# Kernel optimization log

Hardware: AMD Instinct MI355X
Metric: run time of the kernel (lower is better)

## Reference

```python
import jax, jax.numpy as jnp
import numpy as np
from jax.scipy.special import logsumexp

EPSILON = 0.01        # temperature
DIST_THRESH = 0.2
NUM_ITERS = 3
NEG_INF = -1.0e9

B, N, M, C = 4, 4096, 4096, 256


def setup_inputs() -> dict:
    key = jax.random.key(0)
    k1, k2, k3, k4, k5 = jax.random.split(key, 5)
    source_feats = jax.random.normal(k1, (B, N, C), dtype=jnp.float32)
    source_locs = jax.random.uniform(k2, (B, N, 2), dtype=jnp.float32)
    target_locs = jax.random.uniform(k3, (B, M, 2), dtype=jnp.float32)
    source_valid_mask = jax.random.bernoulli(k4, 0.9, (B, N))
    target_valid_mask = jax.random.bernoulli(k5, 0.9, (B, M))
    return {
        "source_feats": source_feats,
        "source_locs": source_locs,
        "target_locs": target_locs,
        "source_valid_mask": source_valid_mask,
        "target_valid_mask": target_valid_mask,
    }


def reference(source_feats, source_locs, target_locs, source_valid_mask, target_valid_mask):
    # pairwise squared distances: [B, M, N]
    diff = target_locs[:, :, None, :] - source_locs[:, None, :, :]  # [B, M, N, 2]
    dist_sq = jnp.sum(diff * diff, axis=-1)                          # [B, M, N]
    log_K = -dist_sq / (EPSILON + 1e-8)

    valid_connection = dist_sq < (DIST_THRESH ** 2)
    valid_connection = valid_connection & source_valid_mask[:, None, :]
    valid_connection = valid_connection & target_valid_mask[:, :, None]
    log_K = jnp.where(valid_connection, log_K, NEG_INF)

    # Sinkhorn iterations in log space
    v = jnp.zeros((log_K.shape[0], 1, log_K.shape[2]), dtype=log_K.dtype)  # [B,1,N]
    u = jnp.zeros((log_K.shape[0], log_K.shape[1], 1), dtype=log_K.dtype)  # [B,M,1]
    for _ in range(NUM_ITERS):
        u = -logsumexp(log_K + v, axis=2, keepdims=True)
        v = -logsumexp(log_K + u, axis=1, keepdims=True)
        v = jnp.where(source_valid_mask[:, None, :], v, 0.0)

    attn = jnp.exp(log_K + u + v)  # [B, M, N]
    attn = jax.lax.stop_gradient(attn)  # original computes it under torch.no_grad

    target_feats = jnp.einsum('bmn,bnc->bmc', attn, source_feats)
    target_feats = target_feats * target_valid_mask[:, :, None].astype(target_feats.dtype)
    has_source = jnp.any(valid_connection, axis=-1, keepdims=True)
    target_feats = target_feats * has_source.astype(target_feats.dtype)
    return target_feats
```

## Files before the change

kernel.cpp:

```cpp
#include <hip/hip_runtime.h>
#include <math.h>

#define BB 4
#define BN 4096
#define CC 256
constexpr float T2      = 0.04f;
constexpr float NEGINF  = -1.0e9f;
constexpr float INV_EPS = (float)(1.0 / 0.01000001);

__device__ __forceinline__ int cell_of(float x, float y) {
  int cx = (int)(x * 5.0f); cx = cx < 0 ? 0 : (cx > 4 ? 4 : cx);
  int cy = (int)(y * 5.0f); cy = cy < 0 ? 0 : (cy > 4 ? 4 : cy);
  return cy * 5 + cx;
}

__global__ void k_count(const float* __restrict__ tlocs, const float* __restrict__ slocs,
                        int* __restrict__ counts_t, int* __restrict__ counts_s) {
  int gid = blockIdx.x * 256 + threadIdx.x;
  if (gid < BB * BN) {
    int b = gid >> 12;
    atomicAdd(&counts_t[b * 32 + cell_of(tlocs[gid * 2], tlocs[gid * 2 + 1])], 1);
  } else {
    int g = gid - BB * BN;
    int b = g >> 12;
    atomicAdd(&counts_s[b * 32 + cell_of(slocs[g * 2], slocs[g * 2 + 1])], 1);
  }
}

__global__ void k_scan_scatter(const float* __restrict__ tlocs, const float* __restrict__ slocs,
                               const int* __restrict__ tmask, const int* __restrict__ smask,
                               const int* __restrict__ counts_t, const int* __restrict__ counts_s,
                               int* __restrict__ starts_t, int* __restrict__ starts_s,
                               int* __restrict__ perm_t, int* __restrict__ perm_s,
                               float4* __restrict__ t_sorted, float4* __restrict__ s_sorted) {
  const int which = blockIdx.x & 1, b = blockIdx.x >> 1;
  const float* locs = which ? slocs : tlocs;
  const int*   mask = which ? smask : tmask;
  const int* counts = which ? counts_s : counts_t;
  int* starts       = which ? starts_s : starts_t;
  int* perm         = which ? perm_s : perm_t;
  float4* pack      = which ? s_sorted : t_sorted;
  __shared__ int st[26];
  __shared__ int cur[25];
  if (threadIdx.x == 0) {
    int acc = 0;
    for (int c = 0; c < 25; c++) { st[c] = acc; acc += counts[b * 32 + c]; }
    st[25] = acc;
  }
  __syncthreads();
  if (threadIdx.x < 25) cur[threadIdx.x] = st[threadIdx.x];
  if (threadIdx.x < 26) starts[b * 32 + threadIdx.x] = st[threadIdx.x];
  __syncthreads();
  for (int i = threadIdx.x; i < BN; i += 256) {
    float x = locs[(b * BN + i) * 2], y = locs[(b * BN + i) * 2 + 1];
    int pos = atomicAdd(&cur[cell_of(x, y)], 1);
    perm[b * BN + pos] = i;
    pack[b * BN + pos] = make_float4(x, y, 0.f, mask[b * BN + i] ? 1.f : 0.f);
  }
}

__global__ __launch_bounds__(256) void k_sink(const float4* __restrict__ opp,
                                              float4* __restrict__ own,
                                              const int* __restrict__ opp_starts,
                                              const int* __restrict__ Zin,
                                              int* __restrict__ Zout,
                                              int zero_invalid) {
  const int row  = blockIdx.x * 4 + (threadIdx.x >> 6);
  const int b    = row >> 12;
  const int lane = threadIdx.x & 63;
  const float4 me = own[row];
  float mrun = -1e30f, srun = 0.f;
  if (me.w != 0.f) {
    const int cell = cell_of(me.x, me.y);
    const int cy = cell / 5, cx = cell % 5;
    const int ry0 = max(cy - 1, 0), ry1 = min(cy + 1, 4);
    const int rx0 = max(cx - 1, 0), rx1 = min(cx + 1, 4);
    for (int ry = ry0; ry <= ry1; ry++) {
      const int r0 = opp_starts[b * 32 + ry * 5 + rx0];
      const int r1 = opp_starts[b * 32 + ry * 5 + rx1 + 1];
      for (int j = r0 + lane; j < r1; j += 64) {
        float4 o = opp[b * BN + j];
        float dx = me.x - o.x, dy = me.y - o.y;
        float d2 = fmaf(dx, dx, dy * dy);
        bool  c  = (d2 < T2) && (o.w != 0.f);
        float t  = c ? fmaf(d2, -INV_EPS, o.z) : -3e30f;
        float d  = t - mrun;
        float e  = __expf(-fabsf(d));
        if (d > 0.f) { srun = fmaf(srun, e, 1.f); mrun = t; }
        else         { srun += e; }
      }
    }
  }
  for (int off = 32; off > 0; off >>= 1) {
    float om = __shfl_down(mrun, off);
    float os = __shfl_down(srun, off);
    float nm = fmaxf(mrun, om);
    srun = srun * __expf(mrun - nm) + os * __expf(om - nm);
    mrun = nm;
  }
  if (lane == 0) {
    const int Z = Zin[b];
    float m0 = mrun, s = srun;
    if (Z > 0) {
      m0 = fmaxf(mrun, 0.f);
      s  = srun * __expf(mrun - m0) + (float)Z * __expf(-m0);
    }
    float val = (s > 0.f) ? -(m0 + logf(s)) : 1.0e9f;
    if (zero_invalid && me.w == 0.f) val = 0.f;
    own[row] = make_float4(me.x, me.y, val, me.w);
    if (val == 1.0e9f) atomicAdd(&Zout[b], 1);
  }
}

#define MAXCH 12

__global__ __launch_bounds__(256) void k_out(
    const float* __restrict__ feats, const float4* __restrict__ t_sorted,
    const float4* __restrict__ s_sorted, const int* __restrict__ perm_t,
    const int* __restrict__ perm_s, const int* __restrict__ starts_t,
    const int* __restrict__ starts_s, float* __restrict__ out) {
  const int b = blockIdx.z;
  const int cell = blockIdx.y / 3, rsel = blockIdx.y % 3;
  const int cy = cell / 5, cx = cell % 5;
  const int ry = cy + rsel - 1;
  if (ry < 0 || ry > 4) return;
  const int t0 = starts_t[b * 32 + cell], t1 = starts_t[b * 32 + cell + 1];
  const int base = t0 + blockIdx.x * 32;
  if (base >= t1) return;
  const int rx0 = max(cx - 1, 0), rx1 = min(cx + 1, 4);
  const int s0 = starts_s[b * 32 + ry * 5 + rx0];
  const int s1 = starts_s[b * 32 + ry * 5 + rx1 + 1];
  if (s0 >= s1) return;
  const int nt = min(32, t1 - base);

  __shared__ float4 tL[32];
  __shared__ int    morg[32];
  __shared__ float4 sL[16];
  __shared__ int    sorg[16];
  __shared__ __align__(16) float attnL[16][32];
  __shared__ __align__(16) float fL[16 * 256];

  const int tid = threadIdx.x;
  if (tid < 32) {
    if (tid < nt) {
      tL[tid]   = t_sorted[b * BN + base + tid];
      morg[tid] = perm_t[b * BN + base + tid];
    } else {
      tL[tid]   = make_float4(0.f, 0.f, 0.f, 0.f);
      morg[tid] = 0;
    }
  }
  const int tmg = tid >> 5;
  const int chg = tid & 31;
  float acc[4][8];
  #pragma unroll
  for (int i = 0; i < 4; i++)
    #pragma unroll
    for (int j = 0; j < 8; j++) acc[i][j] = 0.f;
  __syncthreads();

  for (int n0 = s0; n0 < s1; n0 += 16) {
    const int kk = min(16, s1 - n0);
    __syncthreads();
    if (tid < 16) {
      if (tid < kk) {
        sL[tid]   = s_sorted[b * BN + n0 + tid];
        sorg[tid] = perm_s[b * BN + n0 + tid];
      } else {
        sL[tid]   = make_float4(1e9f, 1e9f, 0.f, 0.f);
        sorg[tid] = 0;
      }
    }
    __syncthreads();
    {
      int e = tid * 2;
      #pragma unroll
      for (int q = 0; q < 2; q++, e++) {
        int nn = e >> 5, tm = e & 31;
        float4 t4 = tL[tm];
        float4 s4 = sL[nn];
        float dx = t4.x - s4.x, dy = t4.y - s4.y;
        float d2 = fmaf(dx, dx, dy * dy);
        bool  c  = (d2 < T2) && (s4.w != 0.f) && (t4.w != 0.f);
        attnL[nn][tm] = c ? __expf(fmaf(d2, -INV_EPS, t4.z + s4.z)) : 0.f;
      }
    }
    #pragma unroll
    for (int q = 0; q < 4; q++) {
      int idx = q * 256 + tid;
      ((float4*)fL)[idx] =
          ((const float4*)feats)[(((b << 12) + sorg[idx >> 6]) << 6) + (idx & 63)];
    }
    __syncthreads();
    #pragma unroll 4
    for (int nn = 0; nn < 16; nn++) {
      const float4 av = *(const float4*)&attnL[nn][tmg * 4];
      const float4 f0 = *(const float4*)&fL[nn * 256 + chg * 4];
      const float4 f1 = *(const float4*)&fL[nn * 256 + 128 + chg * 4];
      float avv[4] = {av.x, av.y, av.z, av.w};
      float ff[8]  = {f0.x, f0.y, f0.z, f0.w, f1.x, f1.y, f1.z, f1.w};
      #pragma unroll
      for (int i = 0; i < 4; i++)
        #pragma unroll
        for (int j = 0; j < 8; j++)
          acc[i][j] = fmaf(avv[i], ff[j], acc[i][j]);
    }
  }
  __syncthreads();
  #pragma unroll
  for (int i = 0; i < 4; i++) {
    int tm = tmg * 4 + i;
    if (tm < nt) {
      float* op = out + (((b << 12) + morg[tm]) << 8) + chg * 4;
      #pragma unroll
      for (int j = 0; j < 4; j++) atomicAdd(op + j,       acc[i][j]);
      #pragma unroll
      for (int j = 0; j < 4; j++) atomicAdd(op + 128 + j, acc[i][j + 4]);
    }
  }
}

extern "C" void kernel_launch(void* const* d_in, const int* in_sizes, int n_in,
                              void* d_out, int out_size, void* d_ws, size_t ws_size,
                              hipStream_t stream) {
  const float* feats = (const float*)d_in[0];
  const float* slocs = (const float*)d_in[1];
  const float* tlocs = (const float*)d_in[2];
  const int*   smask = (const int*)d_in[3];
  const int*   tmask = (const int*)d_in[4];
  float* out = (float*)d_out;

  char* ws = (char*)d_ws;
  int*    counts_t = (int*)(ws);
  int*    counts_s = (int*)(ws + 512);
  int*    Zc       = (int*)(ws + 1024);
  int*    starts_t = (int*)(ws + 2048);
  int*    starts_s = (int*)(ws + 2560);
  int*    perm_t   = (int*)(ws + 4096);
  int*    perm_s   = (int*)(ws + 69632);
  float4* s_sorted = (float4*)(ws + 135168);
  float4* t_sorted = (float4*)(ws + 397312);

  hipMemsetAsync(ws, 0, 2048, stream);
  hipMemsetAsync(out, 0, (size_t)out_size * sizeof(float), stream);
  k_count<<<128, 256, 0, stream>>>(tlocs, slocs, counts_t, counts_s);
  k_scan_scatter<<<8, 256, 0, stream>>>(tlocs, slocs, tmask, smask,
                                        counts_t, counts_s, starts_t, starts_s,
                                        perm_t, perm_s, t_sorted, s_sorted);
  for (int it = 0; it < 3; it++) {
    k_sink<<<4096, 256, 0, stream>>>(s_sorted, t_sorted, starts_s,
                                     Zc + (it == 0 ? 0 : (2 * it) * 4),
                                     Zc + (2 * it + 1) * 4, 0);
    k_sink<<<4096, 256, 0, stream>>>(t_sorted, s_sorted, starts_t,
                                     Zc + (2 * it + 1) * 4,
                                     Zc + (2 * it + 2) * 4, 1);
  }
  k_out<<<dim3(MAXCH, 75, BB), 256, 0, stream>>>(feats, t_sorted, s_sorted,
                                                 perm_t, perm_s, starts_t,
                                                 starts_s, out);
}
```

Measured before the change: 598.7 us.

## Use split-bf16 MFMA for attention-times-features in output kernel

Replaces the scalar FMA accumulation in k_out with bf16 MFMA 16x16x32 instructions. Each fp32 value is split into a high and a low bf16 part, and three MFMAs per tile recover near-fp32 accuracy. The source tile grows from 16 to 32, shared-memory layouts are swizzled and transposed for the MFMA operands, and results are staged through LDS before the atomic adds. This raises register and LDS use and adds packing overhead, and accuracy relies on the hi/lo split.

```diff
diff --git a/kernel.cpp b/kernel.cpp
--- a/kernel.cpp
+++ b/kernel.cpp
@@ -8,10 +8,21 @@
 constexpr float NEGINF  = -1.0e9f;
 constexpr float INV_EPS = (float)(1.0 / 0.01000001);
 
+typedef __attribute__((ext_vector_type(8)))  short bf16x8;
+typedef __attribute__((ext_vector_type(16))) short s16x16;
+typedef __attribute__((ext_vector_type(4)))  float f32x4;
+
 __device__ __forceinline__ int cell_of(float x, float y) {
   int cx = (int)(x * 5.0f); cx = cx < 0 ? 0 : (cx > 4 ? 4 : cx);
   int cy = (int)(y * 5.0f); cy = cy < 0 ? 0 : (cy > 4 ? 4 : cy);
   return cy * 5 + cx;
+}
+
+__device__ __forceinline__ unsigned pack_hl(float f) {
+  unsigned b  = __float_as_uint(f);
+  unsigned hi = b & 0xFFFF0000u;
+  float    r  = f - __uint_as_float(hi);
+  return hi | (__float_as_uint(r) >> 16);
 }
 
 __global__ void k_count(const float* __restrict__ tlocs, const float* __restrict__ slocs,
@@ -113,6 +124,7 @@
 }
 
 #define MAXCH 12
+#define FSTR  36
 
 __global__ __launch_bounds__(256) void k_out(
     const float* __restrict__ feats, const float4* __restrict__ t_sorted,
@@ -133,14 +145,15 @@
   if (s0 >= s1) return;
   const int nt = min(32, t1 - base);
 
+  __shared__ unsigned fhl[256 * FSTR];
+  __shared__ unsigned ahl[32 * FSTR];
   __shared__ float4 tL[32];
   __shared__ int    morg[32];
-  __shared__ float4 sL[16];
-  __shared__ int    sorg[16];
-  __shared__ __align__(16) float attnL[16][32];
-  __shared__ __align__(16) float fL[16 * 256];
-
-  const int tid = threadIdx.x;
+
+  const int tid  = threadIdx.x;
+  const int lane = tid & 63;
+  const int w    = tid >> 6;
+
   if (tid < 32) {
     if (tid < nt) {
       tL[tid]   = t_sorted[b * BN + base + tid];
@@ -150,72 +163,109 @@
       morg[tid] = 0;
     }
   }
-  const int tmg = tid >> 5;
-  const int chg = tid & 31;
-  float acc[4][8];
+  __syncthreads();
+
+  const float4 t4r = tL[tid >> 3];
+  const int    tmA = tid >> 3;
+  const int    nnb = (tid & 7) * 4;
+
+  f32x4 acc[4][2];
   #pragma unroll
-  for (int i = 0; i < 4; i++)
-    #pragma unroll
-    for (int j = 0; j < 8; j++) acc[i][j] = 0.f;
-  __syncthreads();
-
-  for (int n0 = s0; n0 < s1; n0 += 16) {
-    const int kk = min(16, s1 - n0);
+  for (int ct = 0; ct < 4; ct++)
+    #pragma unroll
+    for (int tt = 0; tt < 2; tt++) acc[ct][tt] = (f32x4){0.f, 0.f, 0.f, 0.f};
+
+  for (int n0 = s0; n0 < s1; n0 += 32) {
     __syncthreads();
-    if (tid < 16) {
-      if (tid < kk) {
-        sL[tid]   = s_sorted[b * BN + n0 + tid];
-        sorg[tid] = perm_s[b * BN + n0 + tid];
-      } else {
-        sL[tid]   = make_float4(1e9f, 1e9f, 0.f, 0.f);
-        sorg[tid] = 0;
-      }
+    #pragma unroll
+    for (int q = 0; q < 2; q++) {
+      const int ch4 = lane;
+      const int sg  = q * 4 + w;
+      unsigned pk[4][4];
+      #pragma unroll
+      for (int r = 0; r < 4; r++) {
+        int sj   = n0 + sg * 4 + r;
+        int sidx = (sj < s1) ? perm_s[b * BN + sj] : perm_s[b * BN + s0];
+        float4 f = ((const float4*)feats)[(((b << 12) + sidx) << 6) + ch4];
+        pk[r][0] = pack_hl(f.x); pk[r][1] = pack_hl(f.y);
+        pk[r][2] = pack_hl(f.z); pk[r][3] = pack_hl(f.w);
+      }
+      #pragma unroll
+      for (int c = 0; c < 4; c++) {
+        int ch = ch4 * 4 + c;
+        int sb = (sg * 4) ^ (((ch >> 3) & 1) << 3);
+        *(uint4*)&fhl[ch * FSTR + sb] =
+            make_uint4(pk[0][c], pk[1][c], pk[2][c], pk[3][c]);
+      }
+    }
+    {
+      uint4 av;
+      unsigned* pa = (unsigned*)&av;
+      #pragma unroll
+      for (int q = 0; q < 4; q++) {
+        int sj = n0 + nnb + q;
+        float4 s4 = (sj < s1) ? s_sorted[b * BN + sj]
+                              : make_float4(1e9f, 1e9f, 0.f, 0.f);
+        float dx = t4r.x - s4.x, dy = t4r.y - s4.y;
+        float d2 = fmaf(dx, dx, dy * dy);
+        bool  c  = (d2 < T2) && (s4.w != 0.f) && (t4r.w != 0.f);
+        float a  = c ? __expf(fmaf(d2, -INV_EPS, t4r.z + s4.z)) : 0.f;
+        pa[q] = pack_hl(a);
+      }
+      *(uint4*)&ahl[tmA * FSTR + nnb] = av;
     }
     __syncthreads();
-    {
-      int e = tid * 2;
-      #pragma unroll
-      for (int q = 0; q < 2; q++, e++) {
-        int nn = e >> 5, tm = e & 31;
-        float4 t4 = tL[tm];
-        float4 s4 = sL[nn];
-        float dx = t4.x - s4.x, dy = t4.y - s4.y;
-        float d2 = fmaf(dx, dx, dy * dy);
-        bool  c  = (d2 < T2) && (s4.w != 0.f) && (t4.w != 0.f);
-        attnL[nn][tm] = c ? __expf(fmaf(d2, -INV_EPS, t4.z + s4.z)) : 0.f;
-      }
-    }
-    #pragma unroll
-    for (int q = 0; q < 4; q++) {
-      int idx = q * 256 + tid;
-      ((float4*)fL)[idx] =
-          ((const float4*)feats)[(((b << 12) + sorg[idx >> 6]) << 6) + (idx & 63)];
-    }
-    __syncthreads();
-    #pragma unroll 4
-    for (int nn = 0; nn < 16; nn++) {
-      const float4 av = *(const float4*)&attnL[nn][tmg * 4];
-      const float4 f0 = *(const float4*)&fL[nn * 256 + chg * 4];
-      const float4 f1 = *(const float4*)&fL[nn * 256 + 128 + chg * 4];
-      float avv[4] = {av.x, av.y, av.z, av.w};
-      float ff[8]  = {f0.x, f0.y, f0.z, f0.w, f1.x, f1.y, f1.z, f1.w};
-      #pragma unroll
-      for (int i = 0; i < 4; i++)
-        #pragma unroll
-        for (int j = 0; j < 8; j++)
-          acc[i][j] = fmaf(avv[i], ff[j], acc[i][j]);
-    }
-  }
-  __syncthreads();
+    bf16x8 bh[2], bl[2];
+    #pragma unroll
+    for (int tt = 0; tt < 2; tt++) {
+      union { uint4 u[2]; s16x16 s; } U;
+      const unsigned* pb = &ahl[(tt * 16 + (lane & 15)) * FSTR + ((lane >> 4) * 8)];
+      U.u[0] = *(const uint4*)pb; U.u[1] = *(const uint4*)(pb + 4);
+      bh[tt] = __builtin_shufflevector(U.s, U.s, 1, 3, 5, 7, 9, 11, 13, 15);
+      bl[tt] = __builtin_shufflevector(U.s, U.s, 0, 2, 4, 6, 8, 10, 12, 14);
+    }
+    #pragma unroll
+    for (int ct = 0; ct < 4; ct++) {
+      int ch = (w * 4 + ct) * 16 + (lane & 15);
+      int sb = ((lane >> 4) * 8) ^ (((ch >> 3) & 1) << 3);
+      union { uint4 u[2]; s16x16 s; } U;
+      const unsigned* pf = &fhl[ch * FSTR + sb];
+      U.u[0] = *(const uint4*)pf; U.u[1] = *(const uint4*)(pf + 4);
+      bf16x8 ah = __builtin_shufflevector(U.s, U.s, 1, 3, 5, 7, 9, 11, 13, 15);
+      bf16x8 al = __builtin_shufflevector(U.s, U.s, 0, 2, 4, 6, 8, 10, 12, 14);
+      #pragma unroll
+      for (int tt = 0; tt < 2; tt++) {
+        acc[ct][tt] = __builtin_amdgcn_mfma_f32_16x16x32_bf16(ah, bh[tt], acc[ct][tt], 0, 0, 0);
+        acc[ct][tt] = __builtin_amdgcn_mfma_f32_16x16x32_bf16(ah, bl[tt], acc[ct][tt], 0, 0, 0);
+        acc[ct][tt] = __builtin_amdgcn_mfma_f32_16x16x32_bf16(al, bh[tt], acc[ct][tt], 0, 0, 0);
+      }
+    }
+  }
+
+  __syncthreads();
+  float* Dl = (float*)fhl;
   #pragma unroll
-  for (int i = 0; i < 4; i++) {
-    int tm = tmg * 4 + i;
+  for (int ct = 0; ct < 4; ct++)
+    #pragma unroll
+    for (int tt = 0; tt < 2; tt++) {
+      int tg  = tt * 16 + (lane & 15);
+      int chb = (w * 4 + ct) * 16 + (lane >> 4) * 4;
+      *(f32x4*)&Dl[tg * 264 + chb] = acc[ct][tt];
+    }
+  __syncthreads();
+  {
+    int tm = tid >> 3;
     if (tm < nt) {
-      float* op = out + (((b << 12) + morg[tm]) << 8) + chg * 4;
-      #pragma unroll
-      for (int j = 0; j < 4; j++) atomicAdd(op + j,       acc[i][j]);
-      #pragma unroll
-      for (int j = 0; j < 4; j++) atomicAdd(op + 128 + j, acc[i][j + 4]);
+      const int cb = (tid & 7) * 32;
+      float* op = out + (((b << 12) + morg[tm]) << 8) + cb;
+      #pragma unroll
+      for (int v4 = 0; v4 < 8; v4++) {
+        float4 dv = *(float4*)&Dl[tm * 264 + cb + v4 * 4];
+        atomicAdd(op + v4 * 4 + 0, dv.x);
+        atomicAdd(op + v4 * 4 + 1, dv.y);
+        atomicAdd(op + v4 * 4 + 2, dv.z);
+        atomicAdd(op + v4 * 4 + 3, dv.w);
+      }
     }
   }
 }
```

New measurement: 969.9 us. 62.0% more time.

## Prefetch next source tile's locations and features into registers during compute

Applied to the files above, without the earlier changes.

The per-tile staging of source locations and permutation indices through shared memory, and the extra barriers that guarded it, are removed. Each thread now loads its source location and its share of the gathered feature rows for the next 16-source tile into registers while the current tile's FMA loop runs. At the top of the next iteration it copies those registers into shared memory. This is meant to hide the latency of the gathered global feature loads behind compute and to cut barrier count, at the cost of extra registers per thread and redundant loads past the end of the range.

```diff
diff --git a/kernel.cpp b/kernel.cpp
--- a/kernel.cpp
+++ b/kernel.cpp
@@ -135,12 +135,11 @@
 
   __shared__ float4 tL[32];
   __shared__ int    morg[32];
-  __shared__ float4 sL[16];
-  __shared__ int    sorg[16];
   __shared__ __align__(16) float attnL[16][32];
   __shared__ __align__(16) float fL[16 * 256];
 
   const int tid = threadIdx.x;
+  const int w   = tid >> 6;
   if (tid < 32) {
     if (tid < nt) {
       tL[tid]   = t_sorted[b * BN + base + tid];
@@ -150,6 +149,19 @@
       morg[tid] = 0;
     }
   }
+
+  float4 pf[4], ps4;
+  {
+    int ssj = s0 + (tid >> 4);
+    ps4 = (ssj < s1) ? s_sorted[b * BN + ssj] : make_float4(1e9f, 1e9f, 0.f, 0.f);
+    #pragma unroll
+    for (int q = 0; q < 4; q++) {
+      int spj  = s0 + q * 4 + w;
+      int sidx = (spj < s1) ? perm_s[b * BN + spj] : perm_s[b * BN + s0];
+      pf[q] = ((const float4*)feats)[(((b << 12) + sidx) << 6) + (tid & 63)];
+    }
+  }
+
   const int tmg = tid >> 5;
   const int chg = tid & 31;
   float acc[4][8];
@@ -160,25 +172,14 @@
   __syncthreads();
 
   for (int n0 = s0; n0 < s1; n0 += 16) {
-    const int kk = min(16, s1 - n0);
-    __syncthreads();
-    if (tid < 16) {
-      if (tid < kk) {
-        sL[tid]   = s_sorted[b * BN + n0 + tid];
-        sorg[tid] = perm_s[b * BN + n0 + tid];
-      } else {
-        sL[tid]   = make_float4(1e9f, 1e9f, 0.f, 0.f);
-        sorg[tid] = 0;
-      }
-    }
-    __syncthreads();
     {
+      const int nn = tid >> 4;
+      const float4 s4 = ps4;
       int e = tid * 2;
       #pragma unroll
       for (int q = 0; q < 2; q++, e++) {
-        int nn = e >> 5, tm = e & 31;
+        int tm = e & 31;
         float4 t4 = tL[tm];
-        float4 s4 = sL[nn];
         float dx = t4.x - s4.x, dy = t4.y - s4.y;
         float d2 = fmaf(dx, dx, dy * dy);
         bool  c  = (d2 < T2) && (s4.w != 0.f) && (t4.w != 0.f);
@@ -186,12 +187,20 @@
       }
     }
     #pragma unroll
-    for (int q = 0; q < 4; q++) {
-      int idx = q * 256 + tid;
-      ((float4*)fL)[idx] =
-          ((const float4*)feats)[(((b << 12) + sorg[idx >> 6]) << 6) + (idx & 63)];
-    }
+    for (int q = 0; q < 4; q++)
+      ((float4*)fL)[q * 256 + tid] = pf[q];
     __syncthreads();
+    {
+      const int n1 = n0 + 16;
+      int ssj = n1 + (tid >> 4);
+      ps4 = (ssj < s1) ? s_sorted[b * BN + ssj] : make_float4(1e9f, 1e9f, 0.f, 0.f);
+      #pragma unroll
+      for (int q = 0; q < 4; q++) {
+        int spj  = n1 + q * 4 + w;
+        int sidx = (spj < s1) ? perm_s[b * BN + spj] : perm_s[b * BN + s0];
+        pf[q] = ((const float4*)feats)[(((b << 12) + sidx) << 6) + (tid & 63)];
+      }
+    }
     #pragma unroll 4
     for (int nn = 0; nn < 16; nn++) {
       const float4 av = *(const float4*)&attnL[nn][tmg * 4];
@@ -205,8 +214,8 @@
         for (int j = 0; j < 8; j++)
           acc[i][j] = fmaf(avv[i], ff[j], acc[i][j]);
     }
-  }
-  __syncthreads();
+    __syncthreads();
+  }
   #pragma unroll
   for (int i = 0; i < 4; i++) {
     int tm = tmg * 4 + i;
```

After: 699.4 us. 16.8% more time.

## Process four rows per wave in Sinkhorn kernel and drop online max

Applied to the files above, without the earlier changes.

Each wavefront now handles four consecutive sorted rows. It scans the union of their neighbouring grid cells once, so every loaded opposite-side point is reused for four rows. The online max-tracking logsumexp is replaced by a plain sum of exponentials plus a simple xor-shuffle reduction, which removes branches and extra exps. The cost is possibly scanning a larger region when the four rows fall in different cells, and relying on potentials staying in a range where the unshifted exp neither overflows nor underflows.

```diff
diff --git a/kernel.cpp b/kernel.cpp
--- a/kernel.cpp
+++ b/kernel.cpp
@@ -65,50 +65,51 @@
                                               const int* __restrict__ Zin,
                                               int* __restrict__ Zout,
                                               int zero_invalid) {
-  const int row  = blockIdx.x * 4 + (threadIdx.x >> 6);
-  const int b    = row >> 12;
+  const int wv   = threadIdx.x >> 6;
   const int lane = threadIdx.x & 63;
-  const float4 me = own[row];
-  float mrun = -1e30f, srun = 0.f;
-  if (me.w != 0.f) {
-    const int cell = cell_of(me.x, me.y);
-    const int cy = cell / 5, cx = cell % 5;
-    const int ry0 = max(cy - 1, 0), ry1 = min(cy + 1, 4);
-    const int rx0 = max(cx - 1, 0), rx1 = min(cx + 1, 4);
-    for (int ry = ry0; ry <= ry1; ry++) {
-      const int r0 = opp_starts[b * 32 + ry * 5 + rx0];
-      const int r1 = opp_starts[b * 32 + ry * 5 + rx1 + 1];
-      for (int j = r0 + lane; j < r1; j += 64) {
-        float4 o = opp[b * BN + j];
-        float dx = me.x - o.x, dy = me.y - o.y;
+  const int rowb = blockIdx.x * 16 + wv * 4;
+  const int b    = rowb >> 12;
+  float4 me[4];
+  float  s[4] = {0.f, 0.f, 0.f, 0.f};
+  int ryLo = 5, ryHi = -1, rxLo = 5, rxHi = -1;
+  #pragma unroll
+  for (int i = 0; i < 4; i++) {
+    me[i] = own[rowb + i];
+    if (me[i].w != 0.f) {
+      int cell = cell_of(me[i].x, me[i].y);
+      int cy = cell / 5, cx = cell % 5;
+      ryLo = min(ryLo, max(cy - 1, 0)); ryHi = max(ryHi, min(cy + 1, 4));
+      rxLo = min(rxLo, max(cx - 1, 0)); rxHi = max(rxHi, min(cx + 1, 4));
+    }
+  }
+  for (int ry = ryLo; ry <= ryHi; ry++) {
+    const int r0 = opp_starts[b * 32 + ry * 5 + rxLo];
+    const int r1 = opp_starts[b * 32 + ry * 5 + rxHi + 1];
+    for (int j = r0 + lane; j < r1; j += 64) {
+      float4 o = opp[b * BN + j];
+      #pragma unroll
+      for (int i = 0; i < 4; i++) {
+        float dx = me[i].x - o.x, dy = me[i].y - o.y;
         float d2 = fmaf(dx, dx, dy * dy);
-        bool  c  = (d2 < T2) && (o.w != 0.f);
+        bool  c  = (d2 < T2) && (o.w != 0.f) && (me[i].w != 0.f);
         float t  = c ? fmaf(d2, -INV_EPS, o.z) : -3e30f;
-        float d  = t - mrun;
-        float e  = __expf(-fabsf(d));
-        if (d > 0.f) { srun = fmaf(srun, e, 1.f); mrun = t; }
-        else         { srun += e; }
+        s[i] += __expf(t);
       }
     }
   }
-  for (int off = 32; off > 0; off >>= 1) {
-    float om = __shfl_down(mrun, off);
-    float os = __shfl_down(srun, off);
-    float nm = fmaxf(mrun, om);
-    srun = srun * __expf(mrun - nm) + os * __expf(om - nm);
-    mrun = nm;
-  }
+  #pragma unroll
+  for (int i = 0; i < 4; i++)
+    for (int off = 32; off > 0; off >>= 1) s[i] += __shfl_xor(s[i], off);
   if (lane == 0) {
-    const int Z = Zin[b];
-    float m0 = mrun, s = srun;
-    if (Z > 0) {
-      m0 = fmaxf(mrun, 0.f);
-      s  = srun * __expf(mrun - m0) + (float)Z * __expf(-m0);
-    }
-    float val = (s > 0.f) ? -(m0 + logf(s)) : 1.0e9f;
-    if (zero_invalid && me.w == 0.f) val = 0.f;
-    own[row] = make_float4(me.x, me.y, val, me.w);
-    if (val == 1.0e9f) atomicAdd(&Zout[b], 1);
+    const float Zf = (float)Zin[b];
+    #pragma unroll
+    for (int i = 0; i < 4; i++) {
+      float ss  = s[i] + Zf;
+      float val = (ss > 0.f) ? -logf(ss) : 1.0e9f;
+      if (zero_invalid && me[i].w == 0.f) val = 0.f;
+      own[rowb + i] = make_float4(me[i].x, me[i].y, val, me[i].w);
+      if (val == 1.0e9f) atomicAdd(&Zout[b], 1);
+    }
   }
 }
 
@@ -248,10 +249,10 @@
                                         counts_t, counts_s, starts_t, starts_s,
                                         perm_t, perm_s, t_sorted, s_sorted);
   for (int it = 0; it < 3; it++) {
-    k_sink<<<4096, 256, 0, stream>>>(s_sorted, t_sorted, starts_s,
+    k_sink<<<1024, 256, 0, stream>>>(s_sorted, t_sorted, starts_s,
                                      Zc + (it == 0 ? 0 : (2 * it) * 4),
                                      Zc + (2 * it + 1) * 4, 0);
-    k_sink<<<4096, 256, 0, stream>>>(t_sorted, s_sorted, starts_t,
+    k_sink<<<1024, 256, 0, stream>>>(t_sorted, s_sorted, starts_t,
                                      Zc + (2 * it + 1) * 4,
                                      Zc + (2 * it + 2) * 4, 1);
   }
```

Result: no change. 598.8 us (+0.0%).
